# Performance work log

Hardware: AMD Instinct MI355X
Metric: run time of the kernel (lower is better)

Reference implementation:

```python
import jax, jax.numpy as jnp
import numpy as np

VOCAB, EMBD, H1, H2, OUT = 100000, 128, 256, 128, 1
EPS = 1e-12

def _layernorm(x, g, b):
    mu = jnp.mean(x, axis=-1, keepdims=True)
    var = jnp.mean(jnp.square(x - mu), axis=-1, keepdims=True)
    return (x - mu) * jax.lax.rsqrt(var + EPS) * g + b

def setup_inputs() -> dict:
    key = jax.random.key(0)
    ks = jax.random.split(key, 10)
    B, S = 4096, 50
    return {
        "entity_ids": jax.random.randint(ks[0], (B, S), 0, VOCAB),
        "entity_length": jax.random.randint(ks[1], (B,), 0, S + 1),
        "emb_table": jax.random.normal(ks[2], (VOCAB, EMBD), jnp.float32),
        "ln1_g": jnp.ones((EMBD,), jnp.float32),
        "ln1_b": jnp.zeros((EMBD,), jnp.float32),
        "w1": jax.random.normal(ks[3], (EMBD, H1), jnp.float32) * (1.0 / np.sqrt(EMBD)),
        "b1": jnp.zeros((H1,), jnp.float32),
        "w2": jax.random.normal(ks[4], (H1, H2), jnp.float32) * (1.0 / np.sqrt(H1)),
        "b2": jnp.zeros((H2,), jnp.float32),
        "ln2_g": jnp.ones((H2,), jnp.float32),
        "ln2_b": jnp.zeros((H2,), jnp.float32),
        "fc_w": jax.random.normal(ks[5], (H2, OUT), jnp.float32) * (1.0 / np.sqrt(H2)),
        "fc_b": jnp.zeros((OUT,), jnp.float32),
    }

def reference(entity_ids, entity_length, emb_table, ln1_g, ln1_b, w1, b1, w2, b2, ln2_g, ln2_b, fc_w, fc_b):
    # embed: [B, S, EMBD]
    x = emb_table[entity_ids]
    x = _layernorm(x, ln1_g, ln1_b)
    # MLP (dropout is identity in eval); torch GELU default is exact erf form
    x = jax.nn.gelu(x @ w1 + b1, approximate=False) @ w2 + b2  # [B, S, H2]
    # ragged max-pool over first length positions (length 0 treated as 1)
    lengths = jnp.maximum(entity_length, 1)  # [B]
    S = x.shape[1]
    mask = jnp.arange(S)[None, :] < lengths[:, None]  # [B, S]
    x = jnp.max(jnp.where(mask[:, :, None], x, -jnp.inf), axis=1)  # [B, H2]
    x = _layernorm(x, ln2_g, ln2_b)
    return (x @ fc_w + fc_b).squeeze(-1)  # [B]
```

## Files before the change

### kernel.cpp

```cpp
#include <hip/hip_runtime.h>
#include <hip/hip_bf16.h>
#include <math.h>

typedef __attribute__((ext_vector_type(8))) _Float16 half8;
typedef __attribute__((ext_vector_type(4))) _Float16 half4;
typedef __attribute__((ext_vector_type(4))) float f32x4;

#define EMBD 128
#define H1 256
#define H2 128
#define SLEN 50
#define NROWS 4096
#define MTILE 32
#define DENSE_GRID 768

#define WS_FRAGS    0
#define WS_ROWSTART 131072
#define WS_PACKED   147456
#define WS_PARTIAL  966656

__device__ __forceinline__ float gelu_exact(float h) {
    float ah = fabsf(h);
    float d  = fmaf(0.23163845f, ah, 1.0f);
    float t;
    asm("v_rcp_f32 %0, %1" : "=v"(t) : "v"(d));
    float p = fmaf(1.061405429f, t, -1.453152027f);
    p = fmaf(p, t, 1.421413741f);
    p = fmaf(p, t, -0.284496736f);
    p = fmaf(p, t, 0.254829592f);
    p = p * t;
    float e;
    float x2 = h * h * -0.72134752f;
    asm("v_exp_f32 %0, %1" : "=v"(e) : "v"(x2));
    float er = fmaf(-p, e, 1.0f);
    return fmaf(0.5f * ah, er, 0.5f * h);
}

#define BARRIER_LDS() asm volatile("s_waitcnt lgkmcnt(0)\n\ts_barrier" ::: "memory")

__device__ __forceinline__ int clamp_len(int v) {
    return v < 1 ? 1 : (v > SLEN ? SLEN : v);
}

__global__ __launch_bounds__(256) void setup_kernel(
    const float* __restrict__ w1, const float* __restrict__ w2,
    const int* __restrict__ ids, const int* __restrict__ lens,
    half8* __restrict__ frags, unsigned* __restrict__ packed,
    int* __restrict__ rowstart)
{
    int b = blockIdx.x, t = threadIdx.x;
    if (b < 32) {
        int f = b * 256 + t;
        half8 v;
        if (f < 4096) {
            int fragid = f >> 6, lane = f & 63;
            int kt = fragid >> 4, nt = fragid & 15;
            int col = nt * 16 + (lane & 15);
            int kb  = kt * 32 + (lane >> 4) * 8;
            #pragma unroll
            for (int i = 0; i < 8; ++i) v[i] = (_Float16)w1[(size_t)(kb + i) * H1 + col];
            frags[f] = v;
        } else {
            int f2 = f - 4096;
            int fragid = f2 >> 6, lane = f2 & 63;
            int kt = fragid >> 3, ntc = fragid & 7;
            int col = ntc * 16 + (lane & 15);
            int kb  = kt * 32 + (lane >> 4) * 8;
            #pragma unroll
            for (int i = 0; i < 8; ++i) v[i] = (_Float16)w2[(size_t)(kb + i) * H2 + col];
            frags[4096 + f2] = v;
        }
    } else {
        int lane = t & 63;
        int wv   = t >> 6;
        int start_row = ((b - 32) * 4 + wv) * 64;

        int acc = 0;
        for (int j = lane; j < start_row; j += 64) acc += clamp_len(lens[j]);
        #pragma unroll
        for (int m = 1; m < 64; m <<= 1) acc += __shfl_xor(acc, m, 64);

        int r   = start_row + lane;
        int len = clamp_len(lens[r]);
        int inc = len;
        #pragma unroll
        for (int off = 1; off < 64; off <<= 1) {
            int v = __shfl_up(inc, off, 64);
            if (lane >= off) inc += v;
        }
        int base = acc + inc - len;
        rowstart[r] = base;
        unsigned rtag = (unsigned)r << 17;
        for (int k = 0; k < len; ++k)
            packed[base + k] = (unsigned)ids[r * SLEN + k] | rtag;
    }
}

__global__ __launch_bounds__(512) void dense_kernel(
    const unsigned* __restrict__ packed, const int* __restrict__ rowstart,
    const int* __restrict__ lens,
    const float* __restrict__ emb, const float* __restrict__ ln1g,
    const float* __restrict__ ln1b, const float* __restrict__ b1,
    const float* __restrict__ b2, const half8* __restrict__ wfrag,
    float* __restrict__ partial)
{
    const int tid = threadIdx.x;
    const int w  = tid >> 6;
    const int l  = tid & 63;
    const int ln = l & 15;
    const int lg = l >> 4;
    const int g32 = w * 4 + lg;

    __shared__ __align__(16) _Float16 x_lds[MTILE][EMBD + 8];
    __shared__ __align__(16) _Float16 h1_lds[MTILE][H1 + 8];
    __shared__ unsigned tok_lds[MTILE + 1];
    __shared__ __align__(16) float b1s[H1];
    __shared__ float b2s[H2];

    if (tid < H1) b1s[tid] = b1[tid];
    else if (tid < H1 + H2) b2s[tid - H1] = b2[tid - H1];

    half8 w1r[4][2];
    #pragma unroll
    for (int kt = 0; kt < 4; ++kt)
      #pragma unroll
      for (int j = 0; j < 2; ++j)
        w1r[kt][j] = wfrag[(kt * 16 + w * 2 + j) * 64 + l];
    half8 w2r[8];
    #pragma unroll
    for (int kt = 0; kt < 8; ++kt)
        w2r[kt] = wfrag[4096 + (kt * 8 + w) * 64 + l];

    float g1r[8], b1r[8];
    #pragma unroll
    for (int i = 0; i < 8; ++i) { g1r[i] = ln1g[ln * 8 + i]; b1r[i] = ln1b[ln * 8 + i]; }

    int lastLen = lens[NROWS - 1];
    lastLen = lastLen < 1 ? 1 : (lastLen > SLEN ? SLEN : lastLen);
    const int total = rowstart[NROWS - 1] + lastLen;

    int tile = blockIdx.x;
    int base = tile * MTILE;

    unsigned pkA = 0xFFFFFFFFu, tokA = 0xFFFFFFFFu;
    float4 pa0, pa1; bool vA = false;
    if (base < total) {
        if (base + g32 < total) pkA = packed[base + g32];
        if (tid <= 32) {
            int ti = (tid < 32) ? base + tid : base - 1;
            tokA = (ti >= 0 && ti < total) ? packed[ti] : 0xFFFFFFFFu;
        }
        vA = (pkA != 0xFFFFFFFFu);
        if (vA) {
            const float4* src = (const float4*)(emb + (size_t)(pkA & 0x1FFFFu) * EMBD + ln * 8);
            pa0 = src[0]; pa1 = src[1];
        }
    }

    for (; base < total; tile += (int)gridDim.x, base = tile * MTILE) {
        const int nbase = (tile + (int)gridDim.x) * MTILE;

        if (tid <= 32) tok_lds[tid] = tokA;

        unsigned pkN = 0xFFFFFFFFu, tokN = 0xFFFFFFFFu;
        if (nbase < total) {
            if (nbase + g32 < total) pkN = packed[nbase + g32];
            if (tid <= 32) {
                int ti = (tid < 32) ? nbase + tid : nbase - 1;
                tokN = (ti < total) ? packed[ti] : 0xFFFFFFFFu;
            }
        }

        {
            half8 xo;
            if (vA) {
                float v[8] = {pa0.x, pa0.y, pa0.z, pa0.w, pa1.x, pa1.y, pa1.z, pa1.w};
                float sm = 0.f, ss = 0.f;
                #pragma unroll
                for (int k = 0; k < 8; ++k) { sm += v[k]; ss += v[k] * v[k]; }
                #pragma unroll
                for (int m = 1; m < 16; m <<= 1) {
                    sm += __shfl_xor(sm, m, 64);
                    ss += __shfl_xor(ss, m, 64);
                }
                float mu  = sm * (1.f / 128.f);
                float var = ss * (1.f / 128.f) - mu * mu;
                float rs  = rsqrtf(var + 1e-12f);
                #pragma unroll
                for (int k = 0; k < 8; ++k)
                    xo[k] = (_Float16)((v[k] - mu) * rs * g1r[k] + b1r[k]);
            } else {
                #pragma unroll
                for (int k = 0; k < 8; ++k) xo[k] = (_Float16)0.f;
            }
            *(half8*)&x_lds[g32][ln * 8] = xo;
        }

        BARRIER_LDS();

        f32x4 acc[2][2];
        acc[0][0] = (f32x4){0,0,0,0}; acc[0][1] = (f32x4){0,0,0,0};
        acc[1][0] = (f32x4){0,0,0,0}; acc[1][1] = (f32x4){0,0,0,0};
        #pragma unroll
        for (int kt = 0; kt < 4; ++kt) {
            half8 xf0 = *(const half8*)&x_lds[ln][kt * 32 + lg * 8];
            half8 xf1 = *(const half8*)&x_lds[16 + ln][kt * 32 + lg * 8];
            acc[0][0] = __builtin_amdgcn_mfma_f32_16x16x32_f16(w1r[kt][0], xf0, acc[0][0], 0, 0, 0);
            acc[0][1] = __builtin_amdgcn_mfma_f32_16x16x32_f16(w1r[kt][1], xf0, acc[0][1], 0, 0, 0);
            acc[1][0] = __builtin_amdgcn_mfma_f32_16x16x32_f16(w1r[kt][0], xf1, acc[1][0], 0, 0, 0);
            acc[1][1] = __builtin_amdgcn_mfma_f32_16x16x32_f16(w1r[kt][1], xf1, acc[1][1], 0, 0, 0);
        }

        float4 pb0, pb1; bool vN = (pkN != 0xFFFFFFFFu);
        if (vN) {
            const float4* src = (const float4*)(emb + (size_t)(pkN & 0x1FFFFu) * EMBD + ln * 8);
            pb0 = src[0]; pb1 = src[1];
        }

        #pragma unroll
        for (int m = 0; m < 2; ++m)
          #pragma unroll
          for (int j = 0; j < 2; ++j) {
            f32x4 bb = *(const f32x4*)&b1s[(w * 2 + j) * 16 + lg * 4];
            half4 hv;
            #pragma unroll
            for (int g2 = 0; g2 < 4; ++g2) {
                float h = acc[m][j][g2] + bb[g2];
                hv[g2] = (_Float16)gelu_exact(h);
            }
            *(half4*)&h1_lds[m * 16 + ln][(w * 2 + j) * 16 + lg * 4] = hv;
          }

        int rowj = 0x7FFF, rowp = 0x7FFF;
        if (l < 32) {
            rowj = (int)(tok_lds[l] >> 17);
            rowp = (l == 0) ? (int)(tok_lds[32] >> 17) : (int)(tok_lds[l - 1] >> 17);
        }
        const int prevrow = (int)(tok_lds[32] >> 17);
        bool st = (l < 32) && ((l == 0) || (rowj != rowp));
        unsigned mask = (unsigned)__ballot(st);
        const float b2v = b2s[w * 16 + ln];

        BARRIER_LDS();

        f32x4 acc2[2];
        acc2[0] = (f32x4){0,0,0,0}; acc2[1] = (f32x4){0,0,0,0};
        #pragma unroll
        for (int kt = 0; kt < 8; ++kt) {
            half8 a0 = *(const half8*)&h1_lds[ln][kt * 32 + lg * 8];
            half8 a1 = *(const half8*)&h1_lds[16 + ln][kt * 32 + lg * 8];
            acc2[0] = __builtin_amdgcn_mfma_f32_16x16x32_f16(a0, w2r[kt], acc2[0], 0, 0, 0);
            acc2[1] = __builtin_amdgcn_mfma_f32_16x16x32_f16(a1, w2r[kt], acc2[1], 0, 0, 0);
        }
        float val[2][4];
        #pragma unroll
        for (int m = 0; m < 2; ++m)
          #pragma unroll
          for (int g2 = 0; g2 < 4; ++g2)
            val[m][g2] = acc2[m][g2] + b2v;

        {
            int s0 = 0;
            while (s0 < 32) {
                int s1;
                if (s0 >= 31) s1 = 32;
                else {
                    unsigned m2 = mask >> (s0 + 1);
                    s1 = m2 ? (s0 + __ffs(m2)) : 32;
                }
                int row = __shfl(rowj, s0, 64);
                if (row < NROWS) {
                    float mx = -INFINITY;
                    #pragma unroll
                    for (int m = 0; m < 2; ++m)
                      #pragma unroll
                      for (int g2 = 0; g2 < 4; ++g2) {
                        int tt = m * 16 + lg * 4 + g2;
                        if (tt >= s0 && tt < s1) mx = fmaxf(mx, val[m][g2]);
                      }
                    mx = fmaxf(mx, __shfl_xor(mx, 16, 64));
                    mx = fmaxf(mx, __shfl_xor(mx, 32, 64));
                    int side = (s0 == 0 && row == prevrow) ? 1 + (tile & 1) : 0;
                    if (l < 16)
                        partial[(size_t)row * 384 + side * 128 + w * 16 + l] = mx;
                }
                s0 = s1;
            }
        }

        pkA = pkN; tokA = tokN; vA = vN;
        if (vN) { pa0 = pb0; pa1 = pb1; }
    }
}

__global__ __launch_bounds__(256) void head_kernel(
    const float* __restrict__ partial, const int* __restrict__ rowstart,
    const int* __restrict__ lens, const float* __restrict__ ln2g,
    const float* __restrict__ ln2b, const float* __restrict__ fcw,
    const float* __restrict__ fcb, float* __restrict__ out)
{
    int w = threadIdx.x >> 6, l = threadIdx.x & 63;
    int r = blockIdx.x * 4 + w;
    const float* pr = partial + (size_t)r * 384;

    int start = rowstart[r];
    int len = lens[r]; len = len < 1 ? 1 : (len > SLEN ? SLEN : len);
    int tf = start >> 5, tl = (start + len - 1) >> 5;

    float v0 = pr[l], v1 = pr[64 + l];
    if (tl > tf) {
        int side = 1 + ((tf + 1) & 1);
        v0 = fmaxf(v0, pr[side * 128 + l]);
        v1 = fmaxf(v1, pr[side * 128 + 64 + l]);
    }
    if (tl > tf + 1) {
        int side = 1 + ((tf + 2) & 1);
        v0 = fmaxf(v0, pr[side * 128 + l]);
        v1 = fmaxf(v1, pr[side * 128 + 64 + l]);
    }

    float g2a = ln2g[l], g2c = ln2g[l + 64];
    float b2a = ln2b[l], b2c = ln2b[l + 64];
    float fwa = fcw[l],  fwc = fcw[l + 64];
    float s = v0 + v1, ss = v0 * v0 + v1 * v1;
    #pragma unroll
    for (int m = 1; m < 64; m <<= 1) {
        s  += __shfl_xor(s,  m, 64);
        ss += __shfl_xor(ss, m, 64);
    }
    float mu  = s * (1.f / 128.f);
    float var = ss * (1.f / 128.f) - mu * mu;
    float rs  = rsqrtf(var + 1e-12f);
    float n0 = (v0 - mu) * rs * g2a + b2a;
    float n1 = (v1 - mu) * rs * g2c + b2c;
    float dot = n0 * fwa + n1 * fwc;
    #pragma unroll
    for (int m = 1; m < 64; m <<= 1) dot += __shfl_xor(dot, m, 64);
    if (l == 0) out[r] = dot + fcb[0];
}

extern "C" void kernel_launch(void* const* d_in, const int* in_sizes, int n_in,
                              void* d_out, int out_size, void* d_ws, size_t ws_size,
                              hipStream_t stream) {
    const int*   ids  = (const int*)d_in[0];
    const int*   lens = (const int*)d_in[1];
    const float* emb  = (const float*)d_in[2];
    const float* ln1g = (const float*)d_in[3];
    const float* ln1b = (const float*)d_in[4];
    const float* w1   = (const float*)d_in[5];
    const float* b1   = (const float*)d_in[6];
    const float* w2   = (const float*)d_in[7];
    const float* b2   = (const float*)d_in[8];
    const float* ln2g = (const float*)d_in[9];
    const float* ln2b = (const float*)d_in[10];
    const float* fcw  = (const float*)d_in[11];
    const float* fcb  = (const float*)d_in[12];
    float* out = (float*)d_out;

    char* ws = (char*)d_ws;
    half8*    frags    = (half8*)(ws + WS_FRAGS);
    int*      rowstart = (int*)(ws + WS_ROWSTART);
    unsigned* packed   = (unsigned*)(ws + WS_PACKED);
    float*    partial  = (float*)(ws + WS_PARTIAL);

    hipLaunchKernelGGL(setup_kernel, dim3(48), dim3(256), 0, stream,
                       w1, w2, ids, lens, frags, packed, rowstart);
    hipLaunchKernelGGL(dense_kernel, dim3(DENSE_GRID), dim3(512), 0, stream,
                       packed, rowstart, lens, emb, ln1g, ln1b, b1, b2, frags, partial);
    hipLaunchKernelGGL(head_kernel, dim3(1024), dim3(256), 0, stream,
                       partial, rowstart, lens, ln2g, ln2b, fcw, fcb, out);
}
```

Baseline: 70.92 us.

## Double token tile to 64 rows and shrink partial buffer to two slots

Raises the per-iteration token tile from 32 to 64 rows, so each wave issues twice as many MFMAs per loaded weight fragment and per barrier pair, and lowers the persistent grid to 512 blocks. Because a row of at most 50 tokens can now span at most two 64-token tiles, the partial max buffer drops from three slots to two and the head kernel merges at most one extra slot. This costs more registers and LDS per block and gives fewer blocks, which may reduce occupancy and latency hiding for the embedding gathers.

```diff
diff --git a/kernel.cpp b/kernel.cpp
--- a/kernel.cpp
+++ b/kernel.cpp
@@ -11,8 +11,8 @@
 #define H2 128
 #define SLEN 50
 #define NROWS 4096
-#define MTILE 32
-#define DENSE_GRID 768
+#define MTILE 64
+#define DENSE_GRID 512
 
 #define WS_FRAGS    0
 #define WS_ROWSTART 131072
@@ -135,46 +135,54 @@
     #pragma unroll
     for (int i = 0; i < 8; ++i) { g1r[i] = ln1g[ln * 8 + i]; b1r[i] = ln1b[ln * 8 + i]; }
 
-    int lastLen = lens[NROWS - 1];
-    lastLen = lastLen < 1 ? 1 : (lastLen > SLEN ? SLEN : lastLen);
+    int lastLen = clamp_len(lens[NROWS - 1]);
     const int total = rowstart[NROWS - 1] + lastLen;
 
     int tile = blockIdx.x;
     int base = tile * MTILE;
 
-    unsigned pkA = 0xFFFFFFFFu, tokA = 0xFFFFFFFFu;
-    float4 pa0, pa1; bool vA = false;
+    unsigned pkA[2] = {0xFFFFFFFFu, 0xFFFFFFFFu};
+    unsigned tokA = 0xFFFFFFFFu;
+    float4 pa0[2], pa1[2];
     if (base < total) {
-        if (base + g32 < total) pkA = packed[base + g32];
-        if (tid <= 32) {
-            int ti = (tid < 32) ? base + tid : base - 1;
+        #pragma unroll
+        for (int s = 0; s < 2; ++s)
+            if (base + s * 32 + g32 < total) pkA[s] = packed[base + s * 32 + g32];
+        if (tid <= MTILE) {
+            int ti = (tid < MTILE) ? base + tid : base - 1;
             tokA = (ti >= 0 && ti < total) ? packed[ti] : 0xFFFFFFFFu;
         }
-        vA = (pkA != 0xFFFFFFFFu);
-        if (vA) {
-            const float4* src = (const float4*)(emb + (size_t)(pkA & 0x1FFFFu) * EMBD + ln * 8);
-            pa0 = src[0]; pa1 = src[1];
-        }
+        #pragma unroll
+        for (int s = 0; s < 2; ++s)
+            if (pkA[s] != 0xFFFFFFFFu) {
+                const float4* src = (const float4*)(emb + (size_t)(pkA[s] & 0x1FFFFu) * EMBD + ln * 8);
+                pa0[s] = src[0]; pa1[s] = src[1];
+            }
     }
 
     for (; base < total; tile += (int)gridDim.x, base = tile * MTILE) {
         const int nbase = (tile + (int)gridDim.x) * MTILE;
 
-        if (tid <= 32) tok_lds[tid] = tokA;
-
-        unsigned pkN = 0xFFFFFFFFu, tokN = 0xFFFFFFFFu;
+        if (tid <= MTILE) tok_lds[tid] = tokA;
+
+        unsigned pkN[2] = {0xFFFFFFFFu, 0xFFFFFFFFu};
+        unsigned tokN = 0xFFFFFFFFu;
         if (nbase < total) {
-            if (nbase + g32 < total) pkN = packed[nbase + g32];
-            if (tid <= 32) {
-                int ti = (tid < 32) ? nbase + tid : nbase - 1;
+            #pragma unroll
+            for (int s = 0; s < 2; ++s)
+                if (nbase + s * 32 + g32 < total) pkN[s] = packed[nbase + s * 32 + g32];
+            if (tid <= MTILE) {
+                int ti = (tid < MTILE) ? nbase + tid : nbase - 1;
                 tokN = (ti < total) ? packed[ti] : 0xFFFFFFFFu;
             }
         }
 
-        {
+        #pragma unroll
+        for (int s = 0; s < 2; ++s) {
             half8 xo;
-            if (vA) {
-                float v[8] = {pa0.x, pa0.y, pa0.z, pa0.w, pa1.x, pa1.y, pa1.z, pa1.w};
+            if (pkA[s] != 0xFFFFFFFFu) {
+                float v[8] = {pa0[s].x, pa0[s].y, pa0[s].z, pa0[s].w,
+                              pa1[s].x, pa1[s].y, pa1[s].z, pa1[s].w};
                 float sm = 0.f, ss = 0.f;
                 #pragma unroll
                 for (int k = 0; k < 8; ++k) { sm += v[k]; ss += v[k] * v[k]; }
@@ -193,32 +201,37 @@
                 #pragma unroll
                 for (int k = 0; k < 8; ++k) xo[k] = (_Float16)0.f;
             }
-            *(half8*)&x_lds[g32][ln * 8] = xo;
+            *(half8*)&x_lds[s * 32 + g32][ln * 8] = xo;
         }
 
         BARRIER_LDS();
 
-        f32x4 acc[2][2];
-        acc[0][0] = (f32x4){0,0,0,0}; acc[0][1] = (f32x4){0,0,0,0};
-        acc[1][0] = (f32x4){0,0,0,0}; acc[1][1] = (f32x4){0,0,0,0};
+        f32x4 acc[4][2];
+        #pragma unroll
+        for (int m = 0; m < 4; ++m) { acc[m][0] = (f32x4){0,0,0,0}; acc[m][1] = (f32x4){0,0,0,0}; }
         #pragma unroll
         for (int kt = 0; kt < 4; ++kt) {
-            half8 xf0 = *(const half8*)&x_lds[ln][kt * 32 + lg * 8];
-            half8 xf1 = *(const half8*)&x_lds[16 + ln][kt * 32 + lg * 8];
-            acc[0][0] = __builtin_amdgcn_mfma_f32_16x16x32_f16(w1r[kt][0], xf0, acc[0][0], 0, 0, 0);
-            acc[0][1] = __builtin_amdgcn_mfma_f32_16x16x32_f16(w1r[kt][1], xf0, acc[0][1], 0, 0, 0);
-            acc[1][0] = __builtin_amdgcn_mfma_f32_16x16x32_f16(w1r[kt][0], xf1, acc[1][0], 0, 0, 0);
-            acc[1][1] = __builtin_amdgcn_mfma_f32_16x16x32_f16(w1r[kt][1], xf1, acc[1][1], 0, 0, 0);
-        }
-
-        float4 pb0, pb1; bool vN = (pkN != 0xFFFFFFFFu);
-        if (vN) {
-            const float4* src = (const float4*)(emb + (size_t)(pkN & 0x1FFFFu) * EMBD + ln * 8);
-            pb0 = src[0]; pb1 = src[1];
-        }
-
-        #pragma unroll
-        for (int m = 0; m < 2; ++m)
+            half8 xf[4];
+            #pragma unroll
+            for (int m = 0; m < 4; ++m)
+                xf[m] = *(const half8*)&x_lds[m * 16 + ln][kt * 32 + lg * 8];
+            #pragma unroll
+            for (int m = 0; m < 4; ++m) {
+                acc[m][0] = __builtin_amdgcn_mfma_f32_16x16x32_f16(w1r[kt][0], xf[m], acc[m][0], 0, 0, 0);
+                acc[m][1] = __builtin_amdgcn_mfma_f32_16x16x32_f16(w1r[kt][1], xf[m], acc[m][1], 0, 0, 0);
+            }
+        }
+
+        float4 pb0[2], pb1[2];
+        #pragma unroll
+        for (int s = 0; s < 2; ++s)
+            if (pkN[s] != 0xFFFFFFFFu) {
+                const float4* src = (const float4*)(emb + (size_t)(pkN[s] & 0x1FFFFu) * EMBD + ln * 8);
+                pb0[s] = src[0]; pb1[s] = src[1];
+            }
+
+        #pragma unroll
+        for (int m = 0; m < 4; ++m)
           #pragma unroll
           for (int j = 0; j < 2; ++j) {
             f32x4 bb = *(const f32x4*)&b1s[(w * 2 + j) * 16 + lg * 4];
@@ -231,48 +244,47 @@
             *(half4*)&h1_lds[m * 16 + ln][(w * 2 + j) * 16 + lg * 4] = hv;
           }
 
-        int rowj = 0x7FFF, rowp = 0x7FFF;
-        if (l < 32) {
-            rowj = (int)(tok_lds[l] >> 17);
-            rowp = (l == 0) ? (int)(tok_lds[32] >> 17) : (int)(tok_lds[l - 1] >> 17);
-        }
-        const int prevrow = (int)(tok_lds[32] >> 17);
-        bool st = (l < 32) && ((l == 0) || (rowj != rowp));
-        unsigned mask = (unsigned)__ballot(st);
+        int rowj = (int)(tok_lds[l] >> 17);
+        int rowp = (l == 0) ? (int)(tok_lds[MTILE] >> 17) : (int)(tok_lds[l - 1] >> 17);
+        const int prevrow = (int)(tok_lds[MTILE] >> 17);
+        bool st = (l == 0) || (rowj != rowp);
+        unsigned long long mask = __ballot(st);
         const float b2v = b2s[w * 16 + ln];
 
         BARRIER_LDS();
 
-        f32x4 acc2[2];
-        acc2[0] = (f32x4){0,0,0,0}; acc2[1] = (f32x4){0,0,0,0};
+        f32x4 acc2[4];
+        #pragma unroll
+        for (int m = 0; m < 4; ++m) acc2[m] = (f32x4){0,0,0,0};
         #pragma unroll
         for (int kt = 0; kt < 8; ++kt) {
-            half8 a0 = *(const half8*)&h1_lds[ln][kt * 32 + lg * 8];
-            half8 a1 = *(const half8*)&h1_lds[16 + ln][kt * 32 + lg * 8];
-            acc2[0] = __builtin_amdgcn_mfma_f32_16x16x32_f16(a0, w2r[kt], acc2[0], 0, 0, 0);
-            acc2[1] = __builtin_amdgcn_mfma_f32_16x16x32_f16(a1, w2r[kt], acc2[1], 0, 0, 0);
-        }
-        float val[2][4];
-        #pragma unroll
-        for (int m = 0; m < 2; ++m)
+            #pragma unroll
+            for (int m = 0; m < 4; ++m) {
+                half8 a = *(const half8*)&h1_lds[m * 16 + ln][kt * 32 + lg * 8];
+                acc2[m] = __builtin_amdgcn_mfma_f32_16x16x32_f16(a, w2r[kt], acc2[m], 0, 0, 0);
+            }
+        }
+        float val[4][4];
+        #pragma unroll
+        for (int m = 0; m < 4; ++m)
           #pragma unroll
           for (int g2 = 0; g2 < 4; ++g2)
             val[m][g2] = acc2[m][g2] + b2v;
 
         {
             int s0 = 0;
-            while (s0 < 32) {
+            while (s0 < MTILE) {
                 int s1;
-                if (s0 >= 31) s1 = 32;
+                if (s0 >= MTILE - 1) s1 = MTILE;
                 else {
-                    unsigned m2 = mask >> (s0 + 1);
-                    s1 = m2 ? (s0 + __ffs(m2)) : 32;
+                    unsigned long long m2 = mask >> (s0 + 1);
+                    s1 = m2 ? (s0 + (int)__ffsll((long long)m2)) : MTILE;
                 }
                 int row = __shfl(rowj, s0, 64);
                 if (row < NROWS) {
                     float mx = -INFINITY;
                     #pragma unroll
-                    for (int m = 0; m < 2; ++m)
+                    for (int m = 0; m < 4; ++m)
                       #pragma unroll
                       for (int g2 = 0; g2 < 4; ++g2) {
                         int tt = m * 16 + lg * 4 + g2;
@@ -280,16 +292,18 @@
                       }
                     mx = fmaxf(mx, __shfl_xor(mx, 16, 64));
                     mx = fmaxf(mx, __shfl_xor(mx, 32, 64));
-                    int side = (s0 == 0 && row == prevrow) ? 1 + (tile & 1) : 0;
+                    int side = (s0 == 0 && row == prevrow) ? 1 : 0;
                     if (l < 16)
-                        partial[(size_t)row * 384 + side * 128 + w * 16 + l] = mx;
+                        partial[(size_t)row * 256 + side * 128 + w * 16 + l] = mx;
                 }
                 s0 = s1;
             }
         }
 
-        pkA = pkN; tokA = tokN; vA = vN;
-        if (vN) { pa0 = pb0; pa1 = pb1; }
+        pkA[0] = pkN[0]; pkA[1] = pkN[1]; tokA = tokN;
+        #pragma unroll
+        for (int s = 0; s < 2; ++s)
+            if (pkN[s] != 0xFFFFFFFFu) { pa0[s] = pb0[s]; pa1[s] = pb1[s]; }
     }
 }
 
@@ -301,22 +315,16 @@
 {
     int w = threadIdx.x >> 6, l = threadIdx.x & 63;
     int r = blockIdx.x * 4 + w;
-    const float* pr = partial + (size_t)r * 384;
+    const float* pr = partial + (size_t)r * 256;
 
     int start = rowstart[r];
     int len = lens[r]; len = len < 1 ? 1 : (len > SLEN ? SLEN : len);
-    int tf = start >> 5, tl = (start + len - 1) >> 5;
+    int tf = start >> 6, tl = (start + len - 1) >> 6;
 
     float v0 = pr[l], v1 = pr[64 + l];
     if (tl > tf) {
-        int side = 1 + ((tf + 1) & 1);
-        v0 = fmaxf(v0, pr[side * 128 + l]);
-        v1 = fmaxf(v1, pr[side * 128 + 64 + l]);
-    }
-    if (tl > tf + 1) {
-        int side = 1 + ((tf + 2) & 1);
-        v0 = fmaxf(v0, pr[side * 128 + l]);
-        v1 = fmaxf(v1, pr[side * 128 + 64 + l]);
+        v0 = fmaxf(v0, pr[128 + l]);
+        v1 = fmaxf(v1, pr[192 + l]);
     }
 
     float g2a = ln2g[l], g2c = ln2g[l + 64];
```

Result: slower. 74.54 us (+5.1%).
